# Kernel optimization log

Hardware: AMD Instinct MI355X
Metric: run time of the kernel (lower is better)

The kernel has to match this reference:

```python
import jax, jax.numpy as jnp
import numpy as np

EPS = 1e-6

def _mlp3(x, Wa, ba, Wb, bb, Wc, bc):
    h = jax.nn.relu(x @ Wa + ba)
    h = jax.nn.relu(h @ Wb + bb)
    return h @ Wc + bc

def setup_inputs() -> dict:
    key = jax.random.key(0)
    ks = jax.random.split(key, 16)
    B, D, C, N = 1024, 1024, 128, 100000
    s = 0.02  # weight scale
    return {
        "query": jax.random.normal(ks[0], (B, D), jnp.float32),
        "W1": jax.random.normal(ks[1], (D, D // 2), jnp.float32) * s,
        "b1": jnp.zeros((D // 2,), jnp.float32),
        "W2": jax.random.normal(ks[2], (D // 2, D // 4), jnp.float32) * s,
        "b2": jnp.zeros((D // 4,), jnp.float32),
        "W3": jax.random.normal(ks[3], (D // 4, C), jnp.float32) * s,
        "b3": jnp.zeros((C,), jnp.float32),
        "keys": jax.random.normal(ks[4], (N, C), jnp.float32),
        "values": jax.random.normal(ks[5], (N, C), jnp.float32),
        "D1w": jax.random.normal(ks[6], (C, D // 4), jnp.float32) * s,
        "D1b": jnp.zeros((D // 4,), jnp.float32),
        "D2w": jax.random.normal(ks[7], (D // 4, D // 2), jnp.float32) * s,
        "D2b": jnp.zeros((D // 2,), jnp.float32),
        "D3w": jax.random.normal(ks[8], (D // 2, D), jnp.float32) * s,
        "D3b": jnp.zeros((D,), jnp.float32),
        "k": 5,
    }

def reference(query, W1, b1, W2, b2, W3, b3, keys, values,
              D1w, D1b, D2w, D2b, D3w, D3b, k):
    # Compress query (FAISS path detaches, so stop_gradient is faithful)
    cq = _mlp3(query, W1, b1, W2, b2, W3, b3)          # [B, C]
    cq = jax.lax.stop_gradient(cq)
    keys_c = jax.lax.stop_gradient(keys)
    vals = jax.lax.stop_gradient(values)               # stored values were .detach()ed
    # Brute-force squared-L2 distances (IndexFlatL2 returns squared L2): [B, N]
    d2 = (jnp.sum(cq * cq, axis=1, keepdims=True)
          + jnp.sum(keys_c * keys_c, axis=1)[None, :]
          - 2.0 * cq @ keys_c.T)
    neg_d, idx = jax.lax.top_k(-d2, k)                 # k nearest, ascending distance
    dist = -neg_d                                      # [B, k]
    w = 1.0 / (dist + EPS)
    w = w / jnp.sum(w, axis=1, keepdims=True)          # [B, k]
    gathered = vals[idx]                               # [B, k, C]
    weighted = jnp.einsum('bk,bkc->bc', w, gathered)   # [B, C]
    retrieved = _mlp3(weighted, D1w, D1b, D2w, D2b, D3w, D3b)  # [B, D]
    confidence = 1.0 / (dist[:, 0] + EPS)              # [B]
    return retrieved, confidence
```

## Files before the change

kernel.cpp:

```cpp
#include <hip/hip_runtime.h>
#include <hip/hip_bf16.h>

#define NKEYS  100000
#define NCH    92
#define CHK    1088
#define TPC    17
#define KPAD   (NCH * CHK)
#define NTILE  (KPAD / 64)
#define BQ     1024
#define EPS_F  1e-6f
#define NCAND  (NCH * 4)
#define BIGF   1e30f

typedef __attribute__((ext_vector_type(8))) short bf16x8;
typedef __attribute__((ext_vector_type(4))) float f32x4;

__device__ __forceinline__ void gl_lds16(const uint4* g, uint4* l) {
    __builtin_amdgcn_global_load_lds((const __attribute__((address_space(1))) void*)g,
                                     (__attribute__((address_space(3))) void*)l, 16, 0, 0);
}
__device__ __forceinline__ unsigned umn(unsigned a, unsigned b) { return a < b ? a : b; }
__device__ __forceinline__ unsigned umx(unsigned a, unsigned b) { return a > b ? a : b; }

__device__ __forceinline__ void ins3u(unsigned (&m)[3], unsigned u) {
    unsigned v1 = umn(m[2], u);
    m[2] = umx(m[1], v1);
    unsigned v2 = umn(m[1], v1);
    m[1] = umx(m[0], v2);
    m[0] = umn(m[0], v2);
}
__device__ __forceinline__ void ins4u(unsigned (&m)[4], unsigned u) {
    unsigned v1 = umn(m[3], u);
    m[3] = umx(m[2], v1);
    unsigned v2 = umn(m[2], v1);
    m[2] = umx(m[1], v2);
    unsigned v3 = umn(m[1], v2);
    m[1] = umx(m[0], v3);
    m[0] = umn(m[0], v3);
}

__device__ __forceinline__ void ins5(float (&d)[5], int (&ix)[5], float nd, int ni) {
    if (nd < d[4]) {
        d[4] = nd; ix[4] = ni;
#pragma unroll
        for (int p = 4; p > 0; --p) {
            if (d[p] < d[p - 1]) {
                float td = d[p]; d[p] = d[p - 1]; d[p - 1] = td;
                int   ti = ix[p]; ix[p] = ix[p - 1]; ix[p - 1] = ti;
            }
        }
    }
}

__global__ __launch_bounds__(256)
void cvt_keys(const float* __restrict__ keys, uint4* __restrict__ img,
              float* __restrict__ kk, float* __restrict__ khalf) {
    const int tid = threadIdx.x;
    const int r = tid >> 2, s = tid & 3;
    const int tile = blockIdx.x;
    const int n = tile * 64 + r;
    const int ct = r >> 4, l15 = r & 15;
    const bool live = (n < NKEYS);
    const float* kp = keys + (size_t)n * 128 + s * 32;
    float ss = 0.f;
    uint4 out[4];
#pragma unroll
    for (int q = 0; q < 4; ++q) {
        float4 a = make_float4(0.f, 0.f, 0.f, 0.f), b = a;
        if (live) { a = *(const float4*)(kp + q * 8); b = *(const float4*)(kp + q * 8 + 4); }
        ss += a.x * a.x + a.y * a.y + a.z * a.z + a.w * a.w
            + b.x * b.x + b.y * b.y + b.z * b.z + b.w * b.w;
        float v[8] = {a.x, a.y, a.z, a.w, b.x, b.y, b.z, b.w};
        ushort h[8];
#pragma unroll
        for (int j = 0; j < 8; ++j) {
            __hip_bfloat16 t = __float2bfloat16(v[j]);
            h[j] = *(ushort*)&t;
        }
        out[q] = make_uint4((uint)h[0] | ((uint)h[1] << 16), (uint)h[2] | ((uint)h[3] << 16),
                            (uint)h[4] | ((uint)h[5] << 16), (uint)h[6] | ((uint)h[7] << 16));
    }
    ss += __shfl_xor(ss, 1, 64);
    ss += __shfl_xor(ss, 2, 64);
    if (s == 0) {
        kk[n]    = live ? ss : BIGF;
        khalf[n] = live ? -0.5f * ss : -BIGF;
    }
#pragma unroll
    for (int q = 0; q < 4; ++q)
        img[(size_t)tile * 1024 + ((ct * 4 + s) * 4 + q) * 16 + l15] = out[q];
}

__global__ __launch_bounds__(256)
void sgemm_part(const float* __restrict__ A, const float* __restrict__ W,
                float* __restrict__ P, int M, int N, int K, int kslice) {
    __shared__ float As[16][68];
    __shared__ float Bs[16][64];
    const int tid = threadIdx.x;
    const int tx = tid & 15, ty = tid >> 4;
    const int m0 = blockIdx.y * 64, n0 = blockIdx.x * 64;
    const int kb = blockIdx.z * kslice, ke = kb + kslice;
    float acc[4][4] = {};
    for (int k0 = kb; k0 < ke; k0 += 16) {
        {
            int m = tid >> 2, k4 = (tid & 3) * 4;
            float4 a = *(const float4*)&A[(size_t)(m0 + m) * K + k0 + k4];
            As[k4 + 0][m] = a.x; As[k4 + 1][m] = a.y;
            As[k4 + 2][m] = a.z; As[k4 + 3][m] = a.w;
        }
        {
            int k = tid >> 4, n4 = (tid & 15) * 4;
            *(float4*)&Bs[k][n4] = *(const float4*)&W[(size_t)(k0 + k) * N + n0 + n4];
        }
        __syncthreads();
#pragma unroll
        for (int kkk = 0; kkk < 16; ++kkk) {
            float4 a4 = *(const float4*)&As[kkk][ty * 4];
            float4 b4 = *(const float4*)&Bs[kkk][tx * 4];
            float av[4] = {a4.x, a4.y, a4.z, a4.w};
            float bv[4] = {b4.x, b4.y, b4.z, b4.w};
#pragma unroll
            for (int i = 0; i < 4; ++i)
#pragma unroll
                for (int j = 0; j < 4; ++j)
                    acc[i][j] = fmaf(av[i], bv[j], acc[i][j]);
        }
        __syncthreads();
    }
    P += (size_t)blockIdx.z * M * N;
#pragma unroll
    for (int i = 0; i < 4; ++i)
        *(float4*)&P[(size_t)(m0 + ty * 4 + i) * N + n0 + tx * 4] =
            make_float4(acc[i][0], acc[i][1], acc[i][2], acc[i][3]);
}

template <int RELU>
__global__ __launch_bounds__(256)
void reduce_bias(const float* __restrict__ P, const float* __restrict__ bias,
                 float* __restrict__ C, int MN, int N, int nP) {
    int i4 = (blockIdx.x * 256 + threadIdx.x) * 4;
    if (i4 >= MN) return;
    float4 s = *(const float4*)&P[i4];
    for (int p = 1; p < nP; ++p) {
        float4 v = *(const float4*)&P[(size_t)p * MN + i4];
        s.x += v.x; s.y += v.y; s.z += v.z; s.w += v.w;
    }
    float4 b = *(const float4*)&bias[i4 % N];
    s.x += b.x; s.y += b.y; s.z += b.z; s.w += b.w;
    if (RELU) {
        s.x = fmaxf(s.x, 0.f); s.y = fmaxf(s.y, 0.f);
        s.z = fmaxf(s.z, 0.f); s.w = fmaxf(s.w, 0.f);
    }
    *(float4*)&C[i4] = s;
}

__global__ __launch_bounds__(256)
void rowsq128(const float* __restrict__ X, float* __restrict__ out, int nrows) {
    int lane = threadIdx.x & 63;
    int row  = blockIdx.x * 4 + (threadIdx.x >> 6);
    if (row >= nrows) return;
    const float* x = X + (size_t)row * 128;
    float a = x[lane], b = x[lane + 64];
    float v = a * a + b * b;
#pragma unroll
    for (int off = 32; off > 0; off >>= 1) v += __shfl_down(v, off, 64);
    if (lane == 0) out[row] = v;
}

__global__ __launch_bounds__(256)
void cvt_bf16_rne(const float* __restrict__ in, ushort* __restrict__ out, int n) {
    int i = (blockIdx.x * 256 + threadIdx.x) * 4;
    if (i >= n) return;
    float4 v = *(const float4*)&in[i];
    __hip_bfloat16 h0 = __float2bfloat16(v.x), h1 = __float2bfloat16(v.y);
    __hip_bfloat16 h2 = __float2bfloat16(v.z), h3 = __float2bfloat16(v.w);
    ushort4 o;
    o.x = *(ushort*)&h0; o.y = *(ushort*)&h1; o.z = *(ushort*)&h2; o.w = *(ushort*)&h3;
    *(ushort4*)&out[i] = o;
}

__global__ __launch_bounds__(256)
void cvt_wT(const float* __restrict__ W, uint4* __restrict__ Wimg, int K, int N) {
    const int ctile = blockIdx.x, p = blockIdx.y;
    const int npan = K >> 6;
#pragma unroll
    for (int it = 0; it < 2; ++it) {
        int c = it * 256 + threadIdx.x;
        int l15 = c & 15, quad = (c >> 4) & 3, s = (c >> 6) & 1, ct = c >> 7;
        int n = ctile * 64 + ct * 16 + l15;
        int k = p * 64 + s * 32 + quad * 8;
        ushort h[8];
#pragma unroll
        for (int j = 0; j < 8; ++j) {
            __hip_bfloat16 t = __float2bfloat16(W[(size_t)(k + j) * N + n]);
            h[j] = *(ushort*)&t;
        }
        Wimg[((size_t)ctile * npan + p) * 512 + c] =
            make_uint4((uint)h[0] | ((uint)h[1] << 16), (uint)h[2] | ((uint)h[3] << 16),
                       (uint)h[4] | ((uint)h[5] << 16), (uint)h[6] | ((uint)h[7] << 16));
    }
}

__global__ __launch_bounds__(256, 3)
void screen_topk(const ushort* __restrict__ qbf, const uint4* __restrict__ img,
                 const float* __restrict__ khalf, int* __restrict__ cand_i) {
    __shared__ uint4 buf[2][1024];
    __shared__ float kls[CHK];
    const int tid = threadIdx.x;
    const int wv = tid >> 6, ln = tid & 63;
    const int quad = ln >> 4, l15 = ln & 15;
    const int m0 = blockIdx.y * 128 + wv * 32;
    const int c0 = blockIdx.x * CHK;
    const int t0 = blockIdx.x * TPC;

    bf16x8 afA[4], afB[4];
    {
        const ushort* qa = qbf + (size_t)(m0 + l15) * 128 + quad * 8;
#pragma unroll
        for (int s = 0; s < 4; ++s) {
            afA[s] = *(const bf16x8*)(qa + 32 * s);
            afB[s] = *(const bf16x8*)(qa + 16 * 128 + 32 * s);
        }
    }
    for (int i = tid; i < CHK; i += 256) kls[i] = khalf[c0 + i];

    unsigned mA[4][3], mB[4][3];
#pragma unroll
    for (int r = 0; r < 4; ++r)
#pragma unroll
        for (int p = 0; p < 3; ++p) { mA[r][p] = 0xFFFFFFFFu; mB[r][p] = 0xFFFFFFFFu; }

#pragma unroll
    for (int it = 0; it < 4; ++it)
        gl_lds16(&img[(size_t)t0 * 1024 + it * 256 + wv * 64 + ln], &buf[0][it * 256 + wv * 64]);
    __syncthreads();

    for (int t = 0; t < TPC; ++t) {
        const int b = t & 1;
        if (t + 1 < TPC) {
#pragma unroll
            for (int it = 0; it < 4; ++it)
                gl_lds16(&img[(size_t)(t0 + t + 1) * 1024 + it * 256 + wv * 64 + ln],
                         &buf[b ^ 1][it * 256 + wv * 64]);
        }
#pragma unroll
        for (int ct = 0; ct < 4; ++ct) {
            const int nl = t * 64 + ct * 16 + l15;
            const float kh = kls[nl];
            f32x4 a0 = {kh, kh, kh, kh}, a1 = {kh, kh, kh, kh};
#pragma unroll
            for (int s = 0; s < 4; ++s) {
                bf16x8 bfr = *(const bf16x8*)&buf[b][(ct * 4 + s) * 64 + ln];
                a0 = __builtin_amdgcn_mfma_f32_16x16x32_bf16(afA[s], bfr, a0, 0, 0, 0);
                a1 = __builtin_amdgcn_mfma_f32_16x16x32_bf16(afB[s], bfr, a1, 0, 0, 0);
            }
#pragma unroll
            for (int r = 0; r < 4; ++r) {
                ins3u(mA[r], (__float_as_uint(a0[r]) & 0xFFFFF800u) | (unsigned)nl);
                ins3u(mB[r], (__float_as_uint(a1[r]) & 0xFFFFF800u) | (unsigned)nl);
            }
        }
        __syncthreads();
    }

#pragma unroll
    for (int set = 0; set < 2; ++set) {
#pragma unroll
        for (int r = 0; r < 4; ++r) {
            unsigned m[4];
#pragma unroll
            for (int p = 0; p < 3; ++p) m[p] = set ? mB[r][p] : mA[r][p];
            m[3] = 0xFFFFFFFFu;
#pragma unroll
            for (int st = 1; st <= 8; st <<= 1) {
                unsigned o[4];
#pragma unroll
                for (int p = 0; p < 4; ++p) o[p] = (unsigned)__shfl_xor((int)m[p], st, 64);
#pragma unroll
                for (int p = 0; p < 4; ++p) ins4u(m, o[p]);
            }
            if (l15 == 0) {
                const int row = m0 + set * 16 + quad * 4 + r;
#pragma unroll
                for (int p = 0; p < 4; ++p)
                    cand_i[((size_t)row * NCH + blockIdx.x) * 4 + p] = c0 + (int)(m[p] & 0x7FFu);
            }
        }
    }
}

__global__ __launch_bounds__(512)
void rerank_gather(const int* __restrict__ cand_i, const float* __restrict__ cq,
                   const float* __restrict__ keysf, const float* __restrict__ qq,
                   const float* __restrict__ kk, const float* __restrict__ values,
                   ushort* __restrict__ wbf, float* __restrict__ conf_out) {
    __shared__ __align__(16) float qs[128];
    __shared__ float ed[NCAND];
    __shared__ int   ei[NCAND];
    __shared__ float w5[5];
    __shared__ int   s5[5];
    __shared__ float confs;
    const int row = blockIdx.x, tid = threadIdx.x;
    const int ln = tid & 63;
    const int qd = tid >> 4;
    const int l15 = tid & 15;
    if (tid < 128) qs[tid] = cq[(size_t)row * 128 + tid];
    for (int c = tid; c < NCAND; c += 512) ei[c] = cand_i[(size_t)row * NCAND + c];
    __syncthreads();
    const float4 qa = *(const float4*)&qs[l15 * 8];
    const float4 qb = *(const float4*)&qs[l15 * 8 + 4];
    const float qqr = qq[row];
#pragma unroll 3
    for (int it = 0; it < (NCAND + 31) / 32; ++it) {
        const int c = qd + it * 32;
        if (c < NCAND) {
            const int idx = ei[c];
            const float* kp = &keysf[(size_t)idx * 128 + l15 * 8];
            const float4 ka = *(const float4*)kp;
            const float4 kb = *(const float4*)(kp + 4);
            float dot = qa.x * ka.x + qa.y * ka.y + qa.z * ka.z + qa.w * ka.w
                      + qb.x * kb.x + qb.y * kb.y + qb.z * kb.z + qb.w * kb.w;
            dot += __shfl_xor(dot, 1, 64);
            dot += __shfl_xor(dot, 2, 64);
            dot += __shfl_xor(dot, 4, 64);
            dot += __shfl_xor(dot, 8, 64);
            if (l15 == 0) ed[c] = qqr + kk[idx] - 2.0f * dot;
        }
    }
    __syncthreads();
    if (tid < 64) {
        float bd[5]; int bi[5];
#pragma unroll
        for (int p = 0; p < 5; ++p) { bd[p] = BIGF; bi[p] = 0; }
        for (int c = ln; c < NCAND; c += 64) ins5(bd, bi, ed[c], ei[c]);
#pragma unroll
        for (int m = 1; m <= 32; m <<= 1) {
            float od[5]; int oi[5];
#pragma unroll
            for (int p = 0; p < 5; ++p) {
                od[p] = __shfl_xor(bd[p], m, 64);
                oi[p] = __shfl_xor(bi[p], m, 64);
            }
#pragma unroll
            for (int p = 0; p < 5; ++p) ins5(bd, bi, od[p], oi[p]);
        }
        if (ln == 0) {
            float ww[5]; float s = 0.f;
#pragma unroll
            for (int p = 0; p < 5; ++p) { ww[p] = 1.0f / (bd[p] + EPS_F); s += ww[p]; }
#pragma unroll
            for (int p = 0; p < 5; ++p) { w5[p] = ww[p] / s; s5[p] = bi[p]; }
            confs = 1.0f / (bd[0] + EPS_F);
        }
    }
    __syncthreads();
    if (tid < 128) {
        float acc = 0.f;
#pragma unroll
        for (int p = 0; p < 5; ++p) acc += w5[p] * values[(size_t)s5[p] * 128 + tid];
        __hip_bfloat16 h = __float2bfloat16(acc);
        wbf[(size_t)row * 128 + tid] = *(ushort*)&h;
    }
    if (tid == 0) conf_out[row] = confs;
}

template <int RELU, int OUTF32>
__global__ __launch_bounds__(256)
void bgemm_bias(const ushort* __restrict__ Abf, const uint4* __restrict__ Wimg,
                const float* __restrict__ bias, void* __restrict__ Cout,
                int M, int N, int K) {
    __shared__ uint4 pan[2][512];
    const int tid = threadIdx.x;
    const int wv = tid >> 6, ln = tid & 63;
    const int quad = ln >> 4, l15 = ln & 15;
    const int n0 = blockIdx.x * 64;
    const int m0 = blockIdx.y * 128 + wv * 32;
    const int ctile = blockIdx.x, npan = K >> 6;
    f32x4 acc[2][4];
#pragma unroll
    for (int s = 0; s < 2; ++s)
#pragma unroll
        for (int c = 0; c < 4; ++c) acc[s][c] = (f32x4){0.f, 0.f, 0.f, 0.f};

#pragma unroll
    for (int it = 0; it < 2; ++it)
        gl_lds16(&Wimg[(size_t)ctile * npan * 512 + it * 256 + wv * 64 + ln],
                 &pan[0][it * 256 + wv * 64]);
    __syncthreads();

    for (int p = 0; p < npan; ++p) {
        const int b = p & 1;
        if (p + 1 < npan) {
#pragma unroll
            for (int it = 0; it < 2; ++it)
                gl_lds16(&Wimg[((size_t)ctile * npan + p + 1) * 512 + it * 256 + wv * 64 + ln],
                         &pan[b ^ 1][it * 256 + wv * 64]);
        }
        const ushort* arow = Abf + (size_t)(m0 + l15) * K + p * 64 + quad * 8;
        bf16x8 afA[2], afB[2];
#pragma unroll
        for (int s = 0; s < 2; ++s) {
            afA[s] = *(const bf16x8*)(arow + s * 32);
            afB[s] = *(const bf16x8*)(arow + (size_t)16 * K + s * 32);
        }
#pragma unroll
        for (int ct = 0; ct < 4; ++ct)
#pragma unroll
            for (int s = 0; s < 2; ++s) {
                bf16x8 bfr = *(const bf16x8*)&pan[b][((ct * 2 + s) * 4 + quad) * 16 + l15];
                acc[0][ct] = __builtin_amdgcn_mfma_f32_16x16x32_bf16(afA[s], bfr, acc[0][ct], 0, 0, 0);
                acc[1][ct] = __builtin_amdgcn_mfma_f32_16x16x32_bf16(afB[s], bfr, acc[1][ct], 0, 0, 0);
            }
        __syncthreads();
    }

#pragma unroll
    for (int ct = 0; ct < 4; ++ct) {
        const int col = n0 + ct * 16 + l15;
        const float bv = bias[col];
#pragma unroll
        for (int set = 0; set < 2; ++set)
#pragma unroll
            for (int r = 0; r < 4; ++r) {
                float v = acc[set][ct][r] + bv;
                if (RELU) v = fmaxf(v, 0.f);
                const int row = m0 + set * 16 + quad * 4 + r;
                if (OUTF32) {
                    ((float*)Cout)[(size_t)row * N + col] = v;
                } else {
                    __hip_bfloat16 h = __float2bfloat16(v);
                    ((ushort*)Cout)[(size_t)row * N + col] = *(ushort*)&h;
                }
            }
    }
}

extern "C" void kernel_launch(void* const* d_in, const int* in_sizes, int n_in,
                              void* d_out, int out_size, void* d_ws, size_t ws_size,
                              hipStream_t stream) {
    const float* query  = (const float*)d_in[0];
    const float* W1     = (const float*)d_in[1];
    const float* b1     = (const float*)d_in[2];
    const float* W2     = (const float*)d_in[3];
    const float* b2     = (const float*)d_in[4];
    const float* W3     = (const float*)d_in[5];
    const float* b3     = (const float*)d_in[6];
    const float* keys   = (const float*)d_in[7];
    const float* values = (const float*)d_in[8];
    const float* D1w    = (const float*)d_in[9];
    const float* D1b    = (const float*)d_in[10];
    const float* D2w    = (const float*)d_in[11];
    const float* D2b    = (const float*)d_in[12];
    const float* D3w    = (const float*)d_in[13];
    const float* D3b    = (const float*)d_in[14];
    float* out = (float*)d_out;

    float*  ws    = (float*)d_ws;
    float*  kk    = ws;
    float*  khalf = ws + 100096;
    float*  qq    = ws + 200192;
    float*  cq    = ws + 201216;
    ushort* qbf   = (ushort*)(ws + 332288);
    float*  h1    = ws + 397824;
    float*  h2    = ws + 922112;
    float*  part  = ws + 1184256;
    uint4*  img   = (uint4*)(ws + 3281408);
    int*    cand  = (int*)part;
    ushort* wbf   = (ushort*)(part + 376832);
    ushort* h3bf  = (ushort*)(part + 442368);
    ushort* h4bf  = (ushort*)(part + 573440);
    uint4*  Wimg1 = (uint4*)(part + 835584);
    uint4*  Wimg2 = (uint4*)(part + 851968);
    uint4*  Wimg3 = (uint4*)(part + 917504);
    float*  conf  = out + 1024 * 1024;

    cvt_keys<<<NTILE, 256, 0, stream>>>(keys, img, kk, khalf);
    sgemm_part<<<dim3(8, 16, 4), 256, 0, stream>>>(query, W1, part, 1024, 512, 1024, 256);
    reduce_bias<1><<<512, 256, 0, stream>>>(part, b1, h1, 1024 * 512, 512, 4);
    sgemm_part<<<dim3(4, 16, 8), 256, 0, stream>>>(h1, W2, part, 1024, 256, 512, 64);
    reduce_bias<1><<<256, 256, 0, stream>>>(part, b2, h2, 1024 * 256, 256, 8);
    sgemm_part<<<dim3(2, 16, 8), 256, 0, stream>>>(h2, W3, part, 1024, 128, 256, 32);
    reduce_bias<0><<<128, 256, 0, stream>>>(part, b3, cq, 1024 * 128, 128, 8);
    cvt_wT<<<dim3(4, 2),  256, 0, stream>>>(D1w, Wimg1, 128, 256);
    cvt_wT<<<dim3(8, 4),  256, 0, stream>>>(D2w, Wimg2, 256, 512);
    cvt_wT<<<dim3(16, 8), 256, 0, stream>>>(D3w, Wimg3, 512, 1024);
    rowsq128<<<256, 256, 0, stream>>>(cq, qq, BQ);
    cvt_bf16_rne<<<128, 256, 0, stream>>>(cq, qbf, BQ * 128);
    screen_topk<<<dim3(NCH, BQ / 128), 256, 0, stream>>>(qbf, img, khalf, cand);
    rerank_gather<<<BQ, 512, 0, stream>>>(cand, cq, keys, qq, kk, values, wbf, conf);
    bgemm_bias<1, 0><<<dim3(4, 8),  256, 0, stream>>>(wbf,  Wimg1, D1b, h3bf, 1024, 256,  128);
    bgemm_bias<1, 0><<<dim3(8, 8),  256, 0, stream>>>(h3bf, Wimg2, D2b, h4bf, 1024, 512,  256);
    bgemm_bias<0, 1><<<dim3(16, 8), 256, 0, stream>>>(h4bf, Wimg3, D3b, out,  1024, 1024, 512);

    (void)in_sizes; (void)n_in; (void)out_size; (void)ws_size;
}
```

Measured before the change: 301.7 us.

## Replace FP32 encoder SGEMMs with split-bf16 MFMA GEMMs

The three encoder-MLP layers move from the split-K FP32 SIMT sgemm plus reduce_bias kernels to the bf16 MFMA GEMM. Activations and weights are split into hi/lo bf16 parts and concatenated along K (hi*hi + lo*hi + hi*lo), keeping roughly FP32 accuracy with three bf16 products. The last layer's epilogue also writes the bf16 query copy, which removes the separate conversion kernel, and screen_topk's occupancy hint rises from 3 to 4 blocks. In exchange, K triples, extra split/conversion launches are added, and the workspace layout is rearranged with aliasing.

```diff
diff --git a/kernel.cpp b/kernel.cpp
--- a/kernel.cpp
+++ b/kernel.cpp
@@ -21,6 +21,10 @@
 }
 __device__ __forceinline__ unsigned umn(unsigned a, unsigned b) { return a < b ? a : b; }
 __device__ __forceinline__ unsigned umx(unsigned a, unsigned b) { return a > b ? a : b; }
+__device__ __forceinline__ ushort bf16bits(float v) {
+    __hip_bfloat16 h = __float2bfloat16(v);
+    return *(ushort*)&h;
+}
 
 __device__ __forceinline__ void ins3u(unsigned (&m)[3], unsigned u) {
     unsigned v1 = umn(m[2], u);
@@ -73,10 +77,7 @@
         float v[8] = {a.x, a.y, a.z, a.w, b.x, b.y, b.z, b.w};
         ushort h[8];
 #pragma unroll
-        for (int j = 0; j < 8; ++j) {
-            __hip_bfloat16 t = __float2bfloat16(v[j]);
-            h[j] = *(ushort*)&t;
-        }
+        for (int j = 0; j < 8; ++j) h[j] = bf16bits(v[j]);
         out[q] = make_uint4((uint)h[0] | ((uint)h[1] << 16), (uint)h[2] | ((uint)h[3] << 16),
                             (uint)h[4] | ((uint)h[5] << 16), (uint)h[6] | ((uint)h[7] << 16));
     }
@@ -92,66 +93,73 @@
 }
 
 __global__ __launch_bounds__(256)
-void sgemm_part(const float* __restrict__ A, const float* __restrict__ W,
-                float* __restrict__ P, int M, int N, int K, int kslice) {
-    __shared__ float As[16][68];
-    __shared__ float Bs[16][64];
-    const int tid = threadIdx.x;
-    const int tx = tid & 15, ty = tid >> 4;
-    const int m0 = blockIdx.y * 64, n0 = blockIdx.x * 64;
-    const int kb = blockIdx.z * kslice, ke = kb + kslice;
-    float acc[4][4] = {};
-    for (int k0 = kb; k0 < ke; k0 += 16) {
-        {
-            int m = tid >> 2, k4 = (tid & 3) * 4;
-            float4 a = *(const float4*)&A[(size_t)(m0 + m) * K + k0 + k4];
-            As[k4 + 0][m] = a.x; As[k4 + 1][m] = a.y;
-            As[k4 + 2][m] = a.z; As[k4 + 3][m] = a.w;
-        }
-        {
-            int k = tid >> 4, n4 = (tid & 15) * 4;
-            *(float4*)&Bs[k][n4] = *(const float4*)&W[(size_t)(k0 + k) * N + n0 + n4];
-        }
-        __syncthreads();
-#pragma unroll
-        for (int kkk = 0; kkk < 16; ++kkk) {
-            float4 a4 = *(const float4*)&As[kkk][ty * 4];
-            float4 b4 = *(const float4*)&Bs[kkk][tx * 4];
-            float av[4] = {a4.x, a4.y, a4.z, a4.w};
-            float bv[4] = {b4.x, b4.y, b4.z, b4.w};
-#pragma unroll
-            for (int i = 0; i < 4; ++i)
-#pragma unroll
-                for (int j = 0; j < 4; ++j)
-                    acc[i][j] = fmaf(av[i], bv[j], acc[i][j]);
-        }
-        __syncthreads();
-    }
-    P += (size_t)blockIdx.z * M * N;
-#pragma unroll
-    for (int i = 0; i < 4; ++i)
-        *(float4*)&P[(size_t)(m0 + ty * 4 + i) * N + n0 + tx * 4] =
-            make_float4(acc[i][0], acc[i][1], acc[i][2], acc[i][3]);
-}
-
-template <int RELU>
-__global__ __launch_bounds__(256)
-void reduce_bias(const float* __restrict__ P, const float* __restrict__ bias,
-                 float* __restrict__ C, int MN, int N, int nP) {
-    int i4 = (blockIdx.x * 256 + threadIdx.x) * 4;
-    if (i4 >= MN) return;
-    float4 s = *(const float4*)&P[i4];
-    for (int p = 1; p < nP; ++p) {
-        float4 v = *(const float4*)&P[(size_t)p * MN + i4];
-        s.x += v.x; s.y += v.y; s.z += v.z; s.w += v.w;
-    }
-    float4 b = *(const float4*)&bias[i4 % N];
-    s.x += b.x; s.y += b.y; s.z += b.z; s.w += b.w;
-    if (RELU) {
-        s.x = fmaxf(s.x, 0.f); s.y = fmaxf(s.y, 0.f);
-        s.z = fmaxf(s.z, 0.f); s.w = fmaxf(s.w, 0.f);
-    }
-    *(float4*)&C[i4] = s;
+void split_a(const float* __restrict__ A, ushort* __restrict__ Ax, int K) {
+    const int row = blockIdx.x;
+    for (int i = threadIdx.x * 4; i < K; i += 1024) {
+        float4 v = *(const float4*)&A[(size_t)row * K + i];
+        float x[4] = {v.x, v.y, v.z, v.w};
+        ushort h[4], l[4];
+#pragma unroll
+        for (int j = 0; j < 4; ++j) {
+            __hip_bfloat16 hb = __float2bfloat16(x[j]);
+            h[j] = *(ushort*)&hb;
+            float hf = __bfloat162float(hb);
+            l[j] = bf16bits(x[j] - hf);
+        }
+        ushort* o = Ax + (size_t)row * 3 * K;
+        *(ushort4*)&o[i]         = make_ushort4(h[0], h[1], h[2], h[3]);
+        *(ushort4*)&o[K + i]     = make_ushort4(l[0], l[1], l[2], l[3]);
+        *(ushort4*)&o[2 * K + i] = make_ushort4(h[0], h[1], h[2], h[3]);
+    }
+}
+
+__global__ __launch_bounds__(256)
+void cvt_wT_split(const float* __restrict__ W, uint4* __restrict__ Wimg,
+                  int Ksrc, int N) {
+    const int ctile = blockIdx.x, p = blockIdx.y;
+    const int npanT = gridDim.y;
+    const int pk = Ksrc >> 6;
+    const int part = p / pk, psrc = p - part * pk;
+#pragma unroll
+    for (int it = 0; it < 2; ++it) {
+        int c = it * 256 + threadIdx.x;
+        int l15 = c & 15, quad = (c >> 4) & 3, s = (c >> 6) & 1, ct = c >> 7;
+        int n = ctile * 64 + ct * 16 + l15;
+        int k = psrc * 64 + s * 32 + quad * 8;
+        ushort h[8];
+#pragma unroll
+        for (int j = 0; j < 8; ++j) {
+            float w = W[(size_t)(k + j) * N + n];
+            __hip_bfloat16 hb = __float2bfloat16(w);
+            if (part < 2) h[j] = *(ushort*)&hb;
+            else {
+                float hf = __bfloat162float(hb);
+                h[j] = bf16bits(w - hf);
+            }
+        }
+        Wimg[((size_t)ctile * npanT + p) * 512 + c] =
+            make_uint4((uint)h[0] | ((uint)h[1] << 16), (uint)h[2] | ((uint)h[3] << 16),
+                       (uint)h[4] | ((uint)h[5] << 16), (uint)h[6] | ((uint)h[7] << 16));
+    }
+}
+
+__global__ __launch_bounds__(256)
+void cvt_wT(const float* __restrict__ W, uint4* __restrict__ Wimg, int K, int N) {
+    const int ctile = blockIdx.x, p = blockIdx.y;
+    const int npan = K >> 6;
+#pragma unroll
+    for (int it = 0; it < 2; ++it) {
+        int c = it * 256 + threadIdx.x;
+        int l15 = c & 15, quad = (c >> 4) & 3, s = (c >> 6) & 1, ct = c >> 7;
+        int n = ctile * 64 + ct * 16 + l15;
+        int k = p * 64 + s * 32 + quad * 8;
+        ushort h[8];
+#pragma unroll
+        for (int j = 0; j < 8; ++j) h[j] = bf16bits(W[(size_t)(k + j) * N + n]);
+        Wimg[((size_t)ctile * npan + p) * 512 + c] =
+            make_uint4((uint)h[0] | ((uint)h[1] << 16), (uint)h[2] | ((uint)h[3] << 16),
+                       (uint)h[4] | ((uint)h[5] << 16), (uint)h[6] | ((uint)h[7] << 16));
+    }
 }
 
 __global__ __launch_bounds__(256)
@@ -167,41 +175,87 @@
     if (lane == 0) out[row] = v;
 }
 
-__global__ __launch_bounds__(256)
-void cvt_bf16_rne(const float* __restrict__ in, ushort* __restrict__ out, int n) {
-    int i = (blockIdx.x * 256 + threadIdx.x) * 4;
-    if (i >= n) return;
-    float4 v = *(const float4*)&in[i];
-    __hip_bfloat16 h0 = __float2bfloat16(v.x), h1 = __float2bfloat16(v.y);
-    __hip_bfloat16 h2 = __float2bfloat16(v.z), h3 = __float2bfloat16(v.w);
-    ushort4 o;
-    o.x = *(ushort*)&h0; o.y = *(ushort*)&h1; o.z = *(ushort*)&h2; o.w = *(ushort*)&h3;
-    *(ushort4*)&out[i] = o;
-}
-
-__global__ __launch_bounds__(256)
-void cvt_wT(const float* __restrict__ W, uint4* __restrict__ Wimg, int K, int N) {
-    const int ctile = blockIdx.x, p = blockIdx.y;
-    const int npan = K >> 6;
-#pragma unroll
-    for (int it = 0; it < 2; ++it) {
-        int c = it * 256 + threadIdx.x;
-        int l15 = c & 15, quad = (c >> 4) & 3, s = (c >> 6) & 1, ct = c >> 7;
-        int n = ctile * 64 + ct * 16 + l15;
-        int k = p * 64 + s * 32 + quad * 8;
-        ushort h[8];
-#pragma unroll
-        for (int j = 0; j < 8; ++j) {
-            __hip_bfloat16 t = __float2bfloat16(W[(size_t)(k + j) * N + n]);
-            h[j] = *(ushort*)&t;
-        }
-        Wimg[((size_t)ctile * npan + p) * 512 + c] =
-            make_uint4((uint)h[0] | ((uint)h[1] << 16), (uint)h[2] | ((uint)h[3] << 16),
-                       (uint)h[4] | ((uint)h[5] << 16), (uint)h[6] | ((uint)h[7] << 16));
-    }
-}
-
-__global__ __launch_bounds__(256, 3)
+template <int EPI>
+__global__ __launch_bounds__(256)
+void bgemm_bias(const ushort* __restrict__ Abf, const uint4* __restrict__ Wimg,
+                const float* __restrict__ bias, void* __restrict__ Cout,
+                ushort* __restrict__ Cout2, int M, int N, int K) {
+    __shared__ uint4 pan[2][512];
+    const int tid = threadIdx.x;
+    const int wv = tid >> 6, ln = tid & 63;
+    const int quad = ln >> 4, l15 = ln & 15;
+    const int n0 = blockIdx.x * 64;
+    const int m0 = blockIdx.y * 128 + wv * 32;
+    const int ctile = blockIdx.x, npan = K >> 6;
+    f32x4 acc[2][4];
+#pragma unroll
+    for (int s = 0; s < 2; ++s)
+#pragma unroll
+        for (int c = 0; c < 4; ++c) acc[s][c] = (f32x4){0.f, 0.f, 0.f, 0.f};
+
+#pragma unroll
+    for (int it = 0; it < 2; ++it)
+        gl_lds16(&Wimg[(size_t)ctile * npan * 512 + it * 256 + wv * 64 + ln],
+                 &pan[0][it * 256 + wv * 64]);
+    __syncthreads();
+
+    for (int p = 0; p < npan; ++p) {
+        const int b = p & 1;
+        if (p + 1 < npan) {
+#pragma unroll
+            for (int it = 0; it < 2; ++it)
+                gl_lds16(&Wimg[((size_t)ctile * npan + p + 1) * 512 + it * 256 + wv * 64 + ln],
+                         &pan[b ^ 1][it * 256 + wv * 64]);
+        }
+        const ushort* arow = Abf + (size_t)(m0 + l15) * K + p * 64 + quad * 8;
+        bf16x8 afA[2], afB[2];
+#pragma unroll
+        for (int s = 0; s < 2; ++s) {
+            afA[s] = *(const bf16x8*)(arow + s * 32);
+            afB[s] = *(const bf16x8*)(arow + (size_t)16 * K + s * 32);
+        }
+#pragma unroll
+        for (int ct = 0; ct < 4; ++ct)
+#pragma unroll
+            for (int s = 0; s < 2; ++s) {
+                bf16x8 bfr = *(const bf16x8*)&pan[b][((ct * 2 + s) * 4 + quad) * 16 + l15];
+                acc[0][ct] = __builtin_amdgcn_mfma_f32_16x16x32_bf16(afA[s], bfr, acc[0][ct], 0, 0, 0);
+                acc[1][ct] = __builtin_amdgcn_mfma_f32_16x16x32_bf16(afB[s], bfr, acc[1][ct], 0, 0, 0);
+            }
+        __syncthreads();
+    }
+
+#pragma unroll
+    for (int ct = 0; ct < 4; ++ct) {
+        const int col = n0 + ct * 16 + l15;
+        const float bv = bias[col];
+#pragma unroll
+        for (int set = 0; set < 2; ++set)
+#pragma unroll
+            for (int r = 0; r < 4; ++r) {
+                float v = acc[set][ct][r] + bv;
+                if (EPI == 0 || EPI == 2) v = fmaxf(v, 0.f);
+                const int row = m0 + set * 16 + quad * 4 + r;
+                if (EPI == 0) {
+                    ((ushort*)Cout)[(size_t)row * N + col] = bf16bits(v);
+                } else if (EPI == 1) {
+                    ((float*)Cout)[(size_t)row * N + col] = v;
+                } else if (EPI == 2) {
+                    __hip_bfloat16 hb = __float2bfloat16(v);
+                    float hf = __bfloat162float(hb);
+                    ushort* o = (ushort*)Cout + (size_t)row * 3 * N;
+                    o[col]         = *(ushort*)&hb;
+                    o[N + col]     = bf16bits(v - hf);
+                    o[2 * N + col] = *(ushort*)&hb;
+                } else {
+                    ((float*)Cout)[(size_t)row * N + col] = v;
+                    Cout2[(size_t)row * N + col] = bf16bits(v);
+                }
+            }
+    }
+}
+
+__global__ __launch_bounds__(256, 4)
 void screen_topk(const ushort* __restrict__ qbf, const uint4* __restrict__ img,
                  const float* __restrict__ khalf, int* __restrict__ cand_i) {
     __shared__ uint4 buf[2][1024];
@@ -358,81 +412,9 @@
         float acc = 0.f;
 #pragma unroll
         for (int p = 0; p < 5; ++p) acc += w5[p] * values[(size_t)s5[p] * 128 + tid];
-        __hip_bfloat16 h = __float2bfloat16(acc);
-        wbf[(size_t)row * 128 + tid] = *(ushort*)&h;
+        wbf[(size_t)row * 128 + tid] = bf16bits(acc);
     }
     if (tid == 0) conf_out[row] = confs;
-}
-
-template <int RELU, int OUTF32>
-__global__ __launch_bounds__(256)
-void bgemm_bias(const ushort* __restrict__ Abf, const uint4* __restrict__ Wimg,
-                const float* __restrict__ bias, void* __restrict__ Cout,
-                int M, int N, int K) {
-    __shared__ uint4 pan[2][512];
-    const int tid = threadIdx.x;
-    const int wv = tid >> 6, ln = tid & 63;
-    const int quad = ln >> 4, l15 = ln & 15;
-    const int n0 = blockIdx.x * 64;
-    const int m0 = blockIdx.y * 128 + wv * 32;
-    const int ctile = blockIdx.x, npan = K >> 6;
-    f32x4 acc[2][4];
-#pragma unroll
-    for (int s = 0; s < 2; ++s)
-#pragma unroll
-        for (int c = 0; c < 4; ++c) acc[s][c] = (f32x4){0.f, 0.f, 0.f, 0.f};
-
-#pragma unroll
-    for (int it = 0; it < 2; ++it)
-        gl_lds16(&Wimg[(size_t)ctile * npan * 512 + it * 256 + wv * 64 + ln],
-                 &pan[0][it * 256 + wv * 64]);
-    __syncthreads();
-
-    for (int p = 0; p < npan; ++p) {
-        const int b = p & 1;
-        if (p + 1 < npan) {
-#pragma unroll
-            for (int it = 0; it < 2; ++it)
-                gl_lds16(&Wimg[((size_t)ctile * npan + p + 1) * 512 + it * 256 + wv * 64 + ln],
-                         &pan[b ^ 1][it * 256 + wv * 64]);
-        }
-        const ushort* arow = Abf + (size_t)(m0 + l15) * K + p * 64 + quad * 8;
-        bf16x8 afA[2], afB[2];
-#pragma unroll
-        for (int s = 0; s < 2; ++s) {
-            afA[s] = *(const bf16x8*)(arow + s * 32);
-            afB[s] = *(const bf16x8*)(arow + (size_t)16 * K + s * 32);
-        }
-#pragma unroll
-        for (int ct = 0; ct < 4; ++ct)
-#pragma unroll
-            for (int s = 0; s < 2; ++s) {
-                bf16x8 bfr = *(const bf16x8*)&pan[b][((ct * 2 + s) * 4 + quad) * 16 + l15];
-                acc[0][ct] = __builtin_amdgcn_mfma_f32_16x16x32_bf16(afA[s], bfr, acc[0][ct], 0, 0, 0);
-                acc[1][ct] = __builtin_amdgcn_mfma_f32_16x16x32_bf16(afB[s], bfr, acc[1][ct], 0, 0, 0);
-            }
-        __syncthreads();
-    }
-
-#pragma unroll
-    for (int ct = 0; ct < 4; ++ct) {
-        const int col = n0 + ct * 16 + l15;
-        const float bv = bias[col];
-#pragma unroll
-        for (int set = 0; set < 2; ++set)
-#pragma unroll
-            for (int r = 0; r < 4; ++r) {
-                float v = acc[set][ct][r] + bv;
-                if (RELU) v = fmaxf(v, 0.f);
-                const int row = m0 + set * 16 + quad * 4 + r;
-                if (OUTF32) {
-                    ((float*)Cout)[(size_t)row * N + col] = v;
-                } else {
-                    __hip_bfloat16 h = __float2bfloat16(v);
-                    ((ushort*)Cout)[(size_t)row * N + col] = *(ushort*)&h;
-                }
-            }
-    }
 }
 
 extern "C" void kernel_launch(void* const* d_in, const int* in_sizes, int n_in,
@@ -461,36 +443,40 @@
     float*  qq    = ws + 200192;
     float*  cq    = ws + 201216;
     ushort* qbf   = (ushort*)(ws + 332288);
-    float*  h1    = ws + 397824;
-    float*  h2    = ws + 922112;
-    float*  part  = ws + 1184256;
-    uint4*  img   = (uint4*)(ws + 3281408);
-    int*    cand  = (int*)part;
-    ushort* wbf   = (ushort*)(part + 376832);
-    ushort* h3bf  = (ushort*)(part + 442368);
-    ushort* h4bf  = (ushort*)(part + 573440);
-    uint4*  Wimg1 = (uint4*)(part + 835584);
-    uint4*  Wimg2 = (uint4*)(part + 851968);
-    uint4*  Wimg3 = (uint4*)(part + 917504);
+    int*    cand  = (int*)(ws + 397824);
+    float*  R     = ws + 774656;
+    ushort* xbig  = (ushort*)R;
+    uint4*  W1img = (uint4*)(R + 1572864);
+    uint4*  W2img = (uint4*)(R + 2359296);
+    uint4*  W3img = (uint4*)(R + 2555904);
+    ushort* h1big = (ushort*)(R + 2605056);
+    ushort* h2big = (ushort*)(R + 3391488);
+    uint4*  img   = (uint4*)R;
+    ushort* wbf   = (ushort*)R;
+    ushort* h3bf  = (ushort*)(R + 65536);
+    ushort* h4bf  = (ushort*)(R + 196608);
+    uint4*  Wimg1 = (uint4*)(R + 458752);
+    uint4*  Wimg2 = (uint4*)(R + 475136);
+    uint4*  Wimg3 = (uint4*)(R + 540672);
     float*  conf  = out + 1024 * 1024;
 
+    split_a<<<1024, 256, 0, stream>>>(query, xbig, 1024);
+    cvt_wT_split<<<dim3(8, 48), 256, 0, stream>>>(W1, W1img, 1024, 512);
+    cvt_wT_split<<<dim3(4, 24), 256, 0, stream>>>(W2, W2img, 512, 256);
+    cvt_wT_split<<<dim3(2, 12), 256, 0, stream>>>(W3, W3img, 256, 128);
+    bgemm_bias<2><<<dim3(8, 8), 256, 0, stream>>>(xbig,  W1img, b1, h1big, nullptr, 1024, 512, 3072);
+    bgemm_bias<2><<<dim3(4, 8), 256, 0, stream>>>(h1big, W2img, b2, h2big, nullptr, 1024, 256, 1536);
+    bgemm_bias<3><<<dim3(2, 8), 256, 0, stream>>>(h2big, W3img, b3, cq,    qbf,     1024, 128, 768);
+    rowsq128<<<256, 256, 0, stream>>>(cq, qq, BQ);
     cvt_keys<<<NTILE, 256, 0, stream>>>(keys, img, kk, khalf);
-    sgemm_part<<<dim3(8, 16, 4), 256, 0, stream>>>(query, W1, part, 1024, 512, 1024, 256);
-    reduce_bias<1><<<512, 256, 0, stream>>>(part, b1, h1, 1024 * 512, 512, 4);
-    sgemm_part<<<dim3(4, 16, 8), 256, 0, stream>>>(h1, W2, part, 1024, 256, 512, 64);
-    reduce_bias<1><<<256, 256, 0, stream>>>(part, b2, h2, 1024 * 256, 256, 8);
-    sgemm_part<<<dim3(2, 16, 8), 256, 0, stream>>>(h2, W3, part, 1024, 128, 256, 32);
-    reduce_bias<0><<<128, 256, 0, stream>>>(part, b3, cq, 1024 * 128, 128, 8);
+    screen_topk<<<dim3(NCH, BQ / 128), 256, 0, stream>>>(qbf, img, khalf, cand);
+    rerank_gather<<<BQ, 512, 0, stream>>>(cand, cq, keys, qq, kk, values, wbf, conf);
     cvt_wT<<<dim3(4, 2),  256, 0, stream>>>(D1w, Wimg1, 128, 256);
     cvt_wT<<<dim3(8, 4),  256, 0, stream>>>(D2w, Wimg2, 256, 512);
     cvt_wT<<<dim3(16, 8), 256, 0, stream>>>(D3w, Wimg3, 512, 1024);
-    rowsq128<<<256, 256, 0, stream>>>(cq, qq, BQ);
-    cvt_bf16_rne<<<128, 256, 0, stream>>>(cq, qbf, BQ * 128);
-    screen_topk<<<dim3(NCH, BQ / 128), 256, 0, stream>>>(qbf, img, khalf, cand);
-    rerank_gather<<<BQ, 512, 0, stream>>>(cand, cq, keys, qq, kk, values, wbf, conf);
-    bgemm_bias<1, 0><<<dim3(4, 8),  256, 0, stream>>>(wbf,  Wimg1, D1b, h3bf, 1024, 256,  128);
-    bgemm_bias<1, 0><<<dim3(8, 8),  256, 0, stream>>>(h3bf, Wimg2, D2b, h4bf, 1024, 512,  256);
-    bgemm_bias<0, 1><<<dim3(16, 8), 256, 0, stream>>>(h4bf, Wimg3, D3b, out,  1024, 1024, 512);
+    bgemm_bias<0><<<dim3(4, 8),  256, 0, stream>>>(wbf,  Wimg1, D1b, h3bf, nullptr, 1024, 256,  128);
+    bgemm_bias<0><<<dim3(8, 8),  256, 0, stream>>>(h3bf, Wimg2, D2b, h4bf, nullptr, 1024, 512,  256);
+    bgemm_bias<1><<<dim3(16, 8), 256, 0, stream>>>(h4bf, Wimg3, D3b, out,  nullptr, 1024, 1024, 512);
 
     (void)in_sizes; (void)n_in; (void)out_size; (void)ws_size;
 }
```

Result: slower. 349.7 us (+15.9%).

## Rebalance screening grid to 128 chunks, 512-thread blocks, keep top-3 per chunk

Applied to the files above, without the earlier changes.

The key screening kernel now splits keys into 128 smaller chunks and uses 512-thread blocks covering 256 queries each, so each loaded key tile is reused by twice as many queries. Each chunk now keeps 3 candidates per query instead of 4, which shrinks the cross-lane merge, the candidate buffer and the rerank work. The workspace is repacked so the key image aliases the MLP scratch region, with launches reordered to match, and rerank clamps padded indices. Keeping fewer candidates per chunk could miss true neighbours when several fall in one chunk.

```diff
diff --git a/kernel.cpp b/kernel.cpp
--- a/kernel.cpp
+++ b/kernel.cpp
@@ -2,14 +2,14 @@
 #include <hip/hip_bf16.h>
 
 #define NKEYS  100000
-#define NCH    92
-#define CHK    1088
-#define TPC    17
+#define NCH    128
+#define CHK    832
+#define TPC    13
 #define KPAD   (NCH * CHK)
 #define NTILE  (KPAD / 64)
 #define BQ     1024
 #define EPS_F  1e-6f
-#define NCAND  (NCH * 4)
+#define NCAND  (NCH * 3)
 #define BIGF   1e30f
 
 typedef __attribute__((ext_vector_type(8))) short bf16x8;
@@ -21,6 +21,10 @@
 }
 __device__ __forceinline__ unsigned umn(unsigned a, unsigned b) { return a < b ? a : b; }
 __device__ __forceinline__ unsigned umx(unsigned a, unsigned b) { return a > b ? a : b; }
+__device__ __forceinline__ ushort bf16bits(float v) {
+    __hip_bfloat16 h = __float2bfloat16(v);
+    return *(ushort*)&h;
+}
 
 __device__ __forceinline__ void ins3u(unsigned (&m)[3], unsigned u) {
     unsigned v1 = umn(m[2], u);
@@ -28,15 +32,6 @@
     unsigned v2 = umn(m[1], v1);
     m[1] = umx(m[0], v2);
     m[0] = umn(m[0], v2);
-}
-__device__ __forceinline__ void ins4u(unsigned (&m)[4], unsigned u) {
-    unsigned v1 = umn(m[3], u);
-    m[3] = umx(m[2], v1);
-    unsigned v2 = umn(m[2], v1);
-    m[2] = umx(m[1], v2);
-    unsigned v3 = umn(m[1], v2);
-    m[1] = umx(m[0], v3);
-    m[0] = umn(m[0], v3);
 }
 
 __device__ __forceinline__ void ins5(float (&d)[5], int (&ix)[5], float nd, int ni) {
@@ -73,10 +68,7 @@
         float v[8] = {a.x, a.y, a.z, a.w, b.x, b.y, b.z, b.w};
         ushort h[8];
 #pragma unroll
-        for (int j = 0; j < 8; ++j) {
-            __hip_bfloat16 t = __float2bfloat16(v[j]);
-            h[j] = *(ushort*)&t;
-        }
+        for (int j = 0; j < 8; ++j) h[j] = bf16bits(v[j]);
         out[q] = make_uint4((uint)h[0] | ((uint)h[1] << 16), (uint)h[2] | ((uint)h[3] << 16),
                             (uint)h[4] | ((uint)h[5] << 16), (uint)h[6] | ((uint)h[7] << 16));
     }
@@ -172,10 +164,8 @@
     int i = (blockIdx.x * 256 + threadIdx.x) * 4;
     if (i >= n) return;
     float4 v = *(const float4*)&in[i];
-    __hip_bfloat16 h0 = __float2bfloat16(v.x), h1 = __float2bfloat16(v.y);
-    __hip_bfloat16 h2 = __float2bfloat16(v.z), h3 = __float2bfloat16(v.w);
     ushort4 o;
-    o.x = *(ushort*)&h0; o.y = *(ushort*)&h1; o.z = *(ushort*)&h2; o.w = *(ushort*)&h3;
+    o.x = bf16bits(v.x); o.y = bf16bits(v.y); o.z = bf16bits(v.z); o.w = bf16bits(v.w);
     *(ushort4*)&out[i] = o;
 }
 
@@ -191,17 +181,14 @@
         int k = p * 64 + s * 32 + quad * 8;
         ushort h[8];
 #pragma unroll
-        for (int j = 0; j < 8; ++j) {
-            __hip_bfloat16 t = __float2bfloat16(W[(size_t)(k + j) * N + n]);
-            h[j] = *(ushort*)&t;
-        }
+        for (int j = 0; j < 8; ++j) h[j] = bf16bits(W[(size_t)(k + j) * N + n]);
         Wimg[((size_t)ctile * npan + p) * 512 + c] =
             make_uint4((uint)h[0] | ((uint)h[1] << 16), (uint)h[2] | ((uint)h[3] << 16),
                        (uint)h[4] | ((uint)h[5] << 16), (uint)h[6] | ((uint)h[7] << 16));
     }
 }
 
-__global__ __launch_bounds__(256, 3)
+__global__ __launch_bounds__(512, 4)
 void screen_topk(const ushort* __restrict__ qbf, const uint4* __restrict__ img,
                  const float* __restrict__ khalf, int* __restrict__ cand_i) {
     __shared__ uint4 buf[2][1024];
@@ -209,7 +196,7 @@
     const int tid = threadIdx.x;
     const int wv = tid >> 6, ln = tid & 63;
     const int quad = ln >> 4, l15 = ln & 15;
-    const int m0 = blockIdx.y * 128 + wv * 32;
+    const int m0 = blockIdx.y * 256 + wv * 32;
     const int c0 = blockIdx.x * CHK;
     const int t0 = blockIdx.x * TPC;
 
@@ -222,7 +209,7 @@
             afB[s] = *(const bf16x8*)(qa + 16 * 128 + 32 * s);
         }
     }
-    for (int i = tid; i < CHK; i += 256) kls[i] = khalf[c0 + i];
+    for (int i = tid; i < CHK; i += 512) kls[i] = khalf[c0 + i];
 
     unsigned mA[4][3], mB[4][3];
 #pragma unroll
@@ -231,17 +218,18 @@
         for (int p = 0; p < 3; ++p) { mA[r][p] = 0xFFFFFFFFu; mB[r][p] = 0xFFFFFFFFu; }
 
 #pragma unroll
-    for (int it = 0; it < 4; ++it)
-        gl_lds16(&img[(size_t)t0 * 1024 + it * 256 + wv * 64 + ln], &buf[0][it * 256 + wv * 64]);
+    for (int it = 0; it < 2; ++it)
+        gl_lds16(&img[(size_t)t0 * 1024 + it * 512 + wv * 64 + ln],
+                 &buf[0][it * 512 + wv * 64]);
     __syncthreads();
 
     for (int t = 0; t < TPC; ++t) {
         const int b = t & 1;
         if (t + 1 < TPC) {
 #pragma unroll
-            for (int it = 0; it < 4; ++it)
-                gl_lds16(&img[(size_t)(t0 + t + 1) * 1024 + it * 256 + wv * 64 + ln],
-                         &buf[b ^ 1][it * 256 + wv * 64]);
+            for (int it = 0; it < 2; ++it)
+                gl_lds16(&img[(size_t)(t0 + t + 1) * 1024 + it * 512 + wv * 64 + ln],
+                         &buf[b ^ 1][it * 512 + wv * 64]);
         }
 #pragma unroll
         for (int ct = 0; ct < 4; ++ct) {
@@ -267,23 +255,22 @@
     for (int set = 0; set < 2; ++set) {
 #pragma unroll
         for (int r = 0; r < 4; ++r) {
-            unsigned m[4];
+            unsigned m[3];
 #pragma unroll
             for (int p = 0; p < 3; ++p) m[p] = set ? mB[r][p] : mA[r][p];
-            m[3] = 0xFFFFFFFFu;
 #pragma unroll
             for (int st = 1; st <= 8; st <<= 1) {
-                unsigned o[4];
-#pragma unroll
-                for (int p = 0; p < 4; ++p) o[p] = (unsigned)__shfl_xor((int)m[p], st, 64);
-#pragma unroll
-                for (int p = 0; p < 4; ++p) ins4u(m, o[p]);
+                unsigned o[3];
+#pragma unroll
+                for (int p = 0; p < 3; ++p) o[p] = (unsigned)__shfl_xor((int)m[p], st, 64);
+#pragma unroll
+                for (int p = 0; p < 3; ++p) ins3u(m, o[p]);
             }
             if (l15 == 0) {
                 const int row = m0 + set * 16 + quad * 4 + r;
 #pragma unroll
-                for (int p = 0; p < 4; ++p)
-                    cand_i[((size_t)row * NCH + blockIdx.x) * 4 + p] = c0 + (int)(m[p] & 0x7FFu);
+                for (int p = 0; p < 3; ++p)
+                    cand_i[((size_t)row * NCH + blockIdx.x) * 3 + p] = c0 + (int)(m[p] & 0x7FFu);
             }
         }
     }
@@ -315,7 +302,8 @@
         const int c = qd + it * 32;
         if (c < NCAND) {
             const int idx = ei[c];
-            const float* kp = &keysf[(size_t)idx * 128 + l15 * 8];
+            const int idc = idx < NKEYS ? idx : NKEYS - 1;
+            const float* kp = &keysf[(size_t)idc * 128 + l15 * 8];
             const float4 ka = *(const float4*)kp;
             const float4 kb = *(const float4*)(kp + 4);
             float dot = qa.x * ka.x + qa.y * ka.y + qa.z * ka.z + qa.w * ka.w
@@ -358,8 +346,7 @@
         float acc = 0.f;
 #pragma unroll
         for (int p = 0; p < 5; ++p) acc += w5[p] * values[(size_t)s5[p] * 128 + tid];
-        __hip_bfloat16 h = __float2bfloat16(acc);
-        wbf[(size_t)row * 128 + tid] = *(ushort*)&h;
+        wbf[(size_t)row * 128 + tid] = bf16bits(acc);
     }
     if (tid == 0) conf_out[row] = confs;
 }
@@ -428,8 +415,7 @@
                 if (OUTF32) {
                     ((float*)Cout)[(size_t)row * N + col] = v;
                 } else {
-                    __hip_bfloat16 h = __float2bfloat16(v);
-                    ((ushort*)Cout)[(size_t)row * N + col] = *(ushort*)&h;
+                    ((ushort*)Cout)[(size_t)row * N + col] = bf16bits(v);
                 }
             }
     }
@@ -457,37 +443,38 @@
 
     float*  ws    = (float*)d_ws;
     float*  kk    = ws;
-    float*  khalf = ws + 100096;
-    float*  qq    = ws + 200192;
-    float*  cq    = ws + 201216;
-    ushort* qbf   = (ushort*)(ws + 332288);
-    float*  h1    = ws + 397824;
-    float*  h2    = ws + 922112;
-    float*  part  = ws + 1184256;
-    uint4*  img   = (uint4*)(ws + 3281408);
-    int*    cand  = (int*)part;
-    ushort* wbf   = (ushort*)(part + 376832);
-    ushort* h3bf  = (ushort*)(part + 442368);
-    ushort* h4bf  = (ushort*)(part + 573440);
-    uint4*  Wimg1 = (uint4*)(part + 835584);
-    uint4*  Wimg2 = (uint4*)(part + 851968);
-    uint4*  Wimg3 = (uint4*)(part + 917504);
+    float*  khalf = ws + 106496;
+    float*  qq    = ws + 212992;
+    float*  cq    = ws + 214016;
+    ushort* qbf   = (ushort*)(ws + 345088);
+    int*    cand  = (int*)(ws + 410624);
+    float*  R     = ws + 803840;
+    float*  part  = R;
+    float*  h1    = R + 2097152;
+    float*  h2    = R + 2621440;
+    uint4*  img   = (uint4*)R;
+    ushort* wbf   = (ushort*)R;
+    ushort* h3bf  = (ushort*)(R + 65536);
+    ushort* h4bf  = (ushort*)(R + 196608);
+    uint4*  Wimg1 = (uint4*)(R + 458752);
+    uint4*  Wimg2 = (uint4*)(R + 475136);
+    uint4*  Wimg3 = (uint4*)(R + 540672);
     float*  conf  = out + 1024 * 1024;
 
-    cvt_keys<<<NTILE, 256, 0, stream>>>(keys, img, kk, khalf);
     sgemm_part<<<dim3(8, 16, 4), 256, 0, stream>>>(query, W1, part, 1024, 512, 1024, 256);
     reduce_bias<1><<<512, 256, 0, stream>>>(part, b1, h1, 1024 * 512, 512, 4);
     sgemm_part<<<dim3(4, 16, 8), 256, 0, stream>>>(h1, W2, part, 1024, 256, 512, 64);
     reduce_bias<1><<<256, 256, 0, stream>>>(part, b2, h2, 1024 * 256, 256, 8);
     sgemm_part<<<dim3(2, 16, 8), 256, 0, stream>>>(h2, W3, part, 1024, 128, 256, 32);
     reduce_bias<0><<<128, 256, 0, stream>>>(part, b3, cq, 1024 * 128, 128, 8);
+    rowsq128<<<256, 256, 0, stream>>>(cq, qq, BQ);
+    cvt_bf16_rne<<<128, 256, 0, stream>>>(cq, qbf, BQ * 128);
+    cvt_keys<<<NTILE, 256, 0, stream>>>(keys, img, kk, khalf);
+    screen_topk<<<dim3(NCH, BQ / 256), 512, 0, stream>>>(qbf, img, khalf, cand);
+    rerank_gather<<<BQ, 512, 0, stream>>>(cand, cq, keys, qq, kk, values, wbf, conf);
     cvt_wT<<<dim3(4, 2),  256, 0, stream>>>(D1w, Wimg1, 128, 256);
     cvt_wT<<<dim3(8, 4),  256, 0, stream>>>(D2w, Wimg2, 256, 512);
     cvt_wT<<<dim3(16, 8), 256, 0, stream>>>(D3w, Wimg3, 512, 1024);
-    rowsq128<<<256, 256, 0, stream>>>(cq, qq, BQ);
-    cvt_bf16_rne<<<128, 256, 0, stream>>>(cq, qbf, BQ * 128);
-    screen_topk<<<dim3(NCH, BQ / 128), 256, 0, stream>>>(qbf, img, khalf, cand);
-    rerank_gather<<<BQ, 512, 0, stream>>>(cand, cq, keys, qq, kk, values, wbf, conf);
     bgemm_bias<1, 0><<<dim3(4, 8),  256, 0, stream>>>(wbf,  Wimg1, D1b, h3bf, 1024, 256,  128);
     bgemm_bias<1, 0><<<dim3(8, 8),  256, 0, stream>>>(h3bf, Wimg2, D2b, h4bf, 1024, 512,  256);
     bgemm_bias<0, 1><<<dim3(16, 8), 256, 0, stream>>>(h4bf, Wimg3, D3b, out,  1024, 1024, 512);
```

Result: no change. 298.4 us (-1.1%).
